# Kernel tuning notes

Measured on AMD Instinct MI355X. Metric: run time of the kernel, lower is better.

The kernel has to match this reference:

```python
import jax, jax.numpy as jnp
import numpy as np
from jax.ops import segment_sum

N = 100000      # nodes
E = 1600000     # edges (avg degree 16)
F_IN = 100      # data.num_features
D1 = 64         # dim1
D2 = 64         # dim2
CONV = 4        # conv_count
FC = 2          # fc_count
G = 500         # graphs in batch


def setup_inputs() -> dict:
    key = jax.random.key(0)
    ks = jax.random.split(key, 16)
    inp = {}
    inp['x'] = jax.random.normal(ks[0], (N, F_IN), dtype=jnp.float32)
    inp['edge_index'] = jax.random.randint(ks[1], (2, E), 0, N, dtype=jnp.int64)
    inp['edge_weight'] = jax.random.uniform(ks[2], (E,), dtype=jnp.float32)
    inp['batch'] = jnp.sort(jax.random.randint(ks[3], (N,), 0, G, dtype=jnp.int64))
    s = 0.05
    inp['lin0_w'] = jax.random.normal(ks[4], (F_IN, D1), dtype=jnp.float32) * s
    inp['lin0_b'] = jnp.zeros((D1,), dtype=jnp.float32)
    inp['conv_w'] = jax.random.normal(ks[5], (CONV, D1, D1), dtype=jnp.float32) * s
    inp['conv_b'] = jnp.zeros((CONV, D1), dtype=jnp.float32)
    inp['lin1_w'] = jax.random.normal(ks[6], (D1, D2), dtype=jnp.float32) * s
    inp['lin1_b'] = jnp.zeros((D2,), dtype=jnp.float32)
    inp['fc_w'] = jax.random.normal(ks[7], (FC, D2, D2), dtype=jnp.float32) * s
    inp['fc_b'] = jnp.zeros((FC, D2), dtype=jnp.float32)
    inp['lin2_w'] = jax.random.normal(ks[8], (D2, 1), dtype=jnp.float32) * s
    inp['lin2_b'] = jnp.zeros((1,), dtype=jnp.float32)
    return inp


def reference(x, edge_index, edge_weight, batch,
              lin0_w, lin0_b, conv_w, conv_b,
              lin1_w, lin1_b, fc_w, fc_b, lin2_w, lin2_b):
    row, col = edge_index[0], edge_index[1]  # source -> target

    # GCN symmetric normalization (add_self_loops=False, so 'improved' is a no-op)
    deg = segment_sum(edge_weight, col, num_segments=N)          # [N]
    dis = jnp.where(deg > 0, jax.lax.rsqrt(deg), 0.0)            # deg^{-1/2}, inf->0
    norm = dis[row] * edge_weight * dis[col]                     # [E]

    out = jax.nn.relu(x @ lin0_w + lin0_b)                       # [N, D1]
    for i in range(CONV):
        h = out @ conv_w[i]                                      # [N, D1]
        msg = h[row] * norm[:, None]                             # gather + scale, [E, D1]
        agg = segment_sum(msg, col, num_segments=N)              # scatter-add, [N, D1]
        out = jax.nn.relu(agg + conv_b[i])

    # global_mean_pool over graph ids
    sums = segment_sum(out, batch, num_segments=G)               # [G, D1]
    cnt = segment_sum(jnp.ones((N,), dtype=out.dtype), batch, num_segments=G)
    pooled = sums / jnp.clip(cnt, 1.0)[:, None]

    out = jax.nn.relu(pooled @ lin1_w + lin1_b)                  # [G, D2]
    for i in range(FC):
        out = jax.nn.relu(out @ fc_w[i] + fc_b[i])
    out = out @ lin2_w + lin2_b                                  # [G, 1]
    return out.reshape(-1)                                       # [G]
```

## Files before the change

### kernel.cpp

```cpp
#include <hip/hip_runtime.h>

#define NN 100000
#define NE 1600000
#define FIN 100
#define D 64
#define NCONV 4
#define NG 500

#define NB 196
#define BSH 9
#define EPB 2048
#define NBLKA ((NE + EPB - 1) / EPB)
#define NSCAN (NB * NBLKA)
#define SB 512
#define NBLKS ((NSCAN + SB - 1) / SB)

#define LSTR 136
#define ASTR 72

typedef unsigned int uint;
typedef unsigned short ushort;
typedef __attribute__((ext_vector_type(8))) short bf16x8;
typedef __attribute__((ext_vector_type(4))) float f32x4;

__device__ inline ushort f2bf(float x) {
    uint u = __float_as_uint(x);
    u += 0x7fffu + ((u >> 16) & 1u);
    return (ushort)(u >> 16);
}
__device__ inline float bflo(uint u) { return __uint_as_float(u << 16); }
__device__ inline float bfhi(uint u) { return __uint_as_float(u & 0xffff0000u); }
__device__ inline float bf2f(ushort s) { return __uint_as_float((uint)s << 16); }

__global__ __launch_bounds__(256) void k_hist(const int* __restrict__ col,
                                              int* __restrict__ ghist) {
    __shared__ int lh[NB];
    int t = threadIdx.x;
    if (t < NB) lh[t] = 0;
    __syncthreads();
    int base = blockIdx.x * EPB;
    #pragma unroll
    for (int i = 0; i < 8; ++i) {
        int e = base + i * 256 + t;
        if (e < NE) atomicAdd(&lh[col[e] >> BSH], 1);
    }
    __syncthreads();
    if (t < NB) ghist[t * NBLKA + blockIdx.x] = lh[t];
}

__global__ __launch_bounds__(SB) void s_scan1(const int* __restrict__ in,
                                              int* __restrict__ out,
                                              int* __restrict__ bsums, int n) {
    __shared__ int sh[SB];
    int t = threadIdx.x, i = blockIdx.x * SB + t;
    int v = (i < n) ? in[i] : 0;
    sh[t] = v;
    __syncthreads();
    for (int off = 1; off < SB; off <<= 1) {
        int u = (t >= off) ? sh[t - off] : 0;
        __syncthreads();
        sh[t] += u;
        __syncthreads();
    }
    if (i < n) out[i] = sh[t] - v;
    if (t == SB - 1) bsums[blockIdx.x] = sh[t];
}

__global__ __launch_bounds__(SB) void s_scan2(int* __restrict__ bsums, int nb) {
    __shared__ int sh[SB];
    int t = threadIdx.x;
    int v = (t < nb) ? bsums[t] : 0;
    sh[t] = v;
    __syncthreads();
    for (int off = 1; off < SB; off <<= 1) {
        int u = (t >= off) ? sh[t - off] : 0;
        __syncthreads();
        sh[t] += u;
        __syncthreads();
    }
    if (t < nb) bsums[t] = sh[t] - v;
}

__global__ __launch_bounds__(SB) void s_scan3(int* __restrict__ out,
                                              const int* __restrict__ bsums, int n) {
    int i = blockIdx.x * SB + threadIdx.x;
    if (i < n) out[i] += bsums[blockIdx.x];
}

__global__ __launch_bounds__(256) void k_scatter(const int* __restrict__ row,
                                                 const int* __restrict__ col,
                                                 const float* __restrict__ ew,
                                                 const int* __restrict__ gscan,
                                                 int2* __restrict__ sorted) {
    __shared__ int lcur[NB];
    int t = threadIdx.x;
    if (t < NB) lcur[t] = gscan[t * NBLKA + blockIdx.x];
    __syncthreads();
    int base = blockIdx.x * EPB;
    #pragma unroll
    for (int i = 0; i < 8; ++i) {
        int e = base + i * 256 + t;
        if (e < NE) {
            int c = col[e];
            int pos = atomicAdd(&lcur[c >> BSH], 1);
            sorted[pos] = make_int2(row[e] | ((c & 511) << 17), __float_as_int(ew[e]));
        }
    }
}

__global__ __launch_bounds__(SB) void k_bcsr(const int2* __restrict__ sorted,
                                             const int* __restrict__ gscan,
                                             int* __restrict__ rowstart,
                                             int2* __restrict__ csr) {
    __shared__ int lcnt[SB];
    __shared__ int lscan[SB];
    int t = threadIdx.x, b = blockIdx.x;
    int base = gscan[b * NBLKA];
    int end  = (b == NB - 1) ? NE : gscan[(b + 1) * NBLKA];
    lcnt[t] = 0;
    __syncthreads();
    for (int e = base + t; e < end; e += SB)
        atomicAdd(&lcnt[sorted[e].x >> 17], 1);
    __syncthreads();
    int v = lcnt[t];
    lscan[t] = v;
    __syncthreads();
    for (int off = 1; off < SB; off <<= 1) {
        int u = (t >= off) ? lscan[t - off] : 0;
        __syncthreads();
        lscan[t] += u;
        __syncthreads();
    }
    int ex = lscan[t] - v;
    int idx = b * SB + t;
    if (idx <= NN) rowstart[idx] = base + ex;
    lcnt[t] = base + ex;
    __syncthreads();
    for (int e = base + t; e < end; e += SB) {
        int2 p = sorted[e];
        int slot = atomicAdd(&lcnt[p.x >> 17], 1);
        csr[slot] = make_int2(p.x & 0x1FFFF, p.y);
    }
}

__global__ __launch_bounds__(256) void k_rowdeg(const int2* __restrict__ csr,
                                                const int* __restrict__ rowstart,
                                                float* __restrict__ dis) {
    int t = threadIdx.x;
    int node = blockIdx.x * 16 + (t >> 4);
    int f = t & 15;
    int e0 = rowstart[node], e1 = rowstart[node + 1];
    float d = 0.f;
    for (int e = e0 + f; e < e1; e += 16) d += __int_as_float(csr[e].y);
    d += __shfl_xor(d, 1);
    d += __shfl_xor(d, 2);
    d += __shfl_xor(d, 4);
    d += __shfl_xor(d, 8);
    if (f == 0) dis[node] = (d > 0.f) ? (1.0f / sqrtf(d)) : 0.f;
}

__global__ __launch_bounds__(256) void k_rownorm(int2* __restrict__ csr,
                                                 const int* __restrict__ rowstart,
                                                 const float* __restrict__ dis) {
    int t = threadIdx.x;
    int node = blockIdx.x * 16 + (t >> 4);
    int f = t & 15;
    int e0 = rowstart[node], e1 = rowstart[node + 1];
    float dc = dis[node];
    for (int e = e0 + f; e < e1; e += 16) {
        int2 p = csr[e];
        float w = dis[p.x] * __int_as_float(p.y) * dc;
        csr[e] = make_int2(p.x, __float_as_int(w));
    }
}

__global__ void k_wsplit(const float* __restrict__ conv_w, ushort* __restrict__ wf) {
    int tid = blockIdx.x * blockDim.x + threadIdx.x;
    int j = tid & 7;
    int lane = (tid >> 3) & 63;
    int kh = (tid >> 9) & 1;
    int ct = (tid >> 10) & 3;
    int l = tid >> 12;
    int k = kh * 32 + (lane >> 4) * 8 + j;
    int n = ct * 16 + (lane & 15);
    float w = conv_w[l * D * D + k * D + n];
    ushort hi = f2bf(w);
    ushort lo = f2bf(w - bf2f(hi));
    int base = (((l * 4 + ct) * 2 + kh) * 2) * 512 + lane * 8 + j;
    wf[base] = hi;
    wf[base + 512] = lo;
}

__global__ void k_wsplit0(const float* __restrict__ w, ushort* __restrict__ wf) {
    int tid = blockIdx.x * blockDim.x + threadIdx.x;
    int j = tid & 7;
    int lane = (tid >> 3) & 63;
    int ks = (tid >> 9) & 3;
    int ct = tid >> 11;
    int k = ks * 32 + (lane >> 4) * 8 + j;
    int n = ct * 16 + (lane & 15);
    float v = (k < FIN) ? w[k * D + n] : 0.f;
    ushort hi = f2bf(v);
    ushort lo = f2bf(v - bf2f(hi));
    int base = ((ct * 4 + ks) * 2) * 512 + lane * 8 + j;
    wf[base] = hi;
    wf[base + 512] = lo;
}

__global__ __launch_bounds__(256) void k_lin0_mfma(const float* __restrict__ x,
                                                   const ushort* __restrict__ wf,
                                                   const float* __restrict__ b,
                                                   ushort* __restrict__ out) {
    __shared__ ushort xhi[64 * LSTR];
    __shared__ ushort xlo[64 * LSTR];
    int t = threadIdx.x;
    int r0 = blockIdx.x * 64;
    for (int i = t; i < 1600; i += 256) {
        int r = i / 25, c4 = i - (i / 25) * 25;
        float4 v = {0.f, 0.f, 0.f, 0.f};
        if (r0 + r < NN)
            v = *reinterpret_cast<const float4*>(&x[(size_t)(r0 + r) * FIN + c4 * 4]);
        int base = r * LSTR + c4 * 4;
        ushort h;
        h = f2bf(v.x); xhi[base + 0] = h; xlo[base + 0] = f2bf(v.x - bf2f(h));
        h = f2bf(v.y); xhi[base + 1] = h; xlo[base + 1] = f2bf(v.y - bf2f(h));
        h = f2bf(v.z); xhi[base + 2] = h; xlo[base + 2] = f2bf(v.z - bf2f(h));
        h = f2bf(v.w); xhi[base + 3] = h; xlo[base + 3] = f2bf(v.w - bf2f(h));
    }
    for (int i = t; i < 64 * 28; i += 256) {
        int r = i / 28, c = FIN + (i - (i / 28) * 28);
        xhi[r * LSTR + c] = 0;
        xlo[r * LSTR + c] = 0;
    }
    __syncthreads();
    int wave = t >> 6, lane = t & 63;
    int lrow = wave * 16 + (lane & 15);
    bf16x8 ahi[4], alo[4];
    #pragma unroll
    for (int ks = 0; ks < 4; ++ks) {
        int off = lrow * LSTR + ks * 32 + (lane >> 4) * 8;
        ahi[ks] = *reinterpret_cast<const bf16x8*>(&xhi[off]);
        alo[ks] = *reinterpret_cast<const bf16x8*>(&xlo[off]);
    }
    float bv[4];
    #pragma unroll
    for (int ct = 0; ct < 4; ++ct) bv[ct] = b[ct * 16 + (lane & 15)];
    int r = r0 + wave * 16;
    f32x4 acc[4];
    #pragma unroll
    for (int ct = 0; ct < 4; ++ct) {
        acc[ct] = {bv[ct], bv[ct], bv[ct], bv[ct]};
        #pragma unroll
        for (int ks = 0; ks < 4; ++ks) {
            int base = ((ct * 4 + ks) * 2) * 512 + lane * 8;
            bf16x8 wh = *reinterpret_cast<const bf16x8*>(&wf[base]);
            bf16x8 wl = *reinterpret_cast<const bf16x8*>(&wf[base + 512]);
            acc[ct] = __builtin_amdgcn_mfma_f32_16x16x32_bf16(ahi[ks], wh, acc[ct], 0, 0, 0);
            acc[ct] = __builtin_amdgcn_mfma_f32_16x16x32_bf16(ahi[ks], wl, acc[ct], 0, 0, 0);
            acc[ct] = __builtin_amdgcn_mfma_f32_16x16x32_bf16(alo[ks], wh, acc[ct], 0, 0, 0);
        }
    }
    #pragma unroll
    for (int ct = 0; ct < 4; ++ct) {
        int ocol = ct * 16 + (lane & 15);
        #pragma unroll
        for (int i = 0; i < 4; ++i) {
            int orow = r + (lane >> 4) * 4 + i;
            if (orow < NN) out[orow * D + ocol] = f2bf(fmaxf(acc[ct][i], 0.f));
        }
    }
}

__global__ __launch_bounds__(256, 8) void k_conv_fused(const ushort* __restrict__ src,
                                                       const int* __restrict__ rowstart,
                                                       const int2* __restrict__ csr,
                                                       const ushort* __restrict__ wf,
                                                       const float* __restrict__ bias,
                                                       ushort* __restrict__ dst) {
    __shared__ ushort arow[16 * ASTR];
    int t = threadIdx.x;
    int wave = t >> 6, lane = t & 63;
    int g = lane >> 4;
    int f = lane & 15;
    int rloc = wave * 4 + g;
    int node = blockIdx.x * 16 + rloc;
    int e0 = rowstart[node], e1 = rowstart[node + 1];
    float4 acc = {0.f, 0.f, 0.f, 0.f};
    int2 p0, p1, p2, p3;
    {
        int a0 = e0 + 0 < e1 ? e0 + 0 : 0;
        int a1 = e0 + 1 < e1 ? e0 + 1 : 0;
        int a2 = e0 + 2 < e1 ? e0 + 2 : 0;
        int a3 = e0 + 3 < e1 ? e0 + 3 : 0;
        p0 = csr[a0]; p1 = csr[a1]; p2 = csr[a2]; p3 = csr[a3];
    }
    for (int base = e0; base < e1; base += 4) {
        int n0 = base + 4 < e1 ? base + 4 : 0;
        int n1 = base + 5 < e1 ? base + 5 : 0;
        int n2 = base + 6 < e1 ? base + 6 : 0;
        int n3 = base + 7 < e1 ? base + 7 : 0;
        int2 q0 = csr[n0], q1 = csr[n1], q2 = csr[n2], q3 = csr[n3];
        float w0 = (base + 0 < e1) ? __int_as_float(p0.y) : 0.f;
        float w1 = (base + 1 < e1) ? __int_as_float(p1.y) : 0.f;
        float w2 = (base + 2 < e1) ? __int_as_float(p2.y) : 0.f;
        float w3 = (base + 3 < e1) ? __int_as_float(p3.y) : 0.f;
        uint2 v0 = *reinterpret_cast<const uint2*>(&src[p0.x * D + f * 4]);
        uint2 v1 = *reinterpret_cast<const uint2*>(&src[p1.x * D + f * 4]);
        uint2 v2 = *reinterpret_cast<const uint2*>(&src[p2.x * D + f * 4]);
        uint2 v3 = *reinterpret_cast<const uint2*>(&src[p3.x * D + f * 4]);
        acc.x = fmaf(bflo(v0.x), w0, acc.x); acc.y = fmaf(bfhi(v0.x), w0, acc.y);
        acc.z = fmaf(bflo(v0.y), w0, acc.z); acc.w = fmaf(bfhi(v0.y), w0, acc.w);
        acc.x = fmaf(bflo(v1.x), w1, acc.x); acc.y = fmaf(bfhi(v1.x), w1, acc.y);
        acc.z = fmaf(bflo(v1.y), w1, acc.z); acc.w = fmaf(bfhi(v1.y), w1, acc.w);
        acc.x = fmaf(bflo(v2.x), w2, acc.x); acc.y = fmaf(bfhi(v2.x), w2, acc.y);
        acc.z = fmaf(bflo(v2.y), w2, acc.z); acc.w = fmaf(bfhi(v2.y), w2, acc.w);
        acc.x = fmaf(bflo(v3.x), w3, acc.x); acc.y = fmaf(bfhi(v3.x), w3, acc.y);
        acc.z = fmaf(bflo(v3.y), w3, acc.z); acc.w = fmaf(bfhi(v3.y), w3, acc.w);
        p0 = q0; p1 = q1; p2 = q2; p3 = q3;
    }
    uint2 o;
    o.x = (uint)f2bf(acc.x) | ((uint)f2bf(acc.y) << 16);
    o.y = (uint)f2bf(acc.z) | ((uint)f2bf(acc.w) << 16);
    *reinterpret_cast<uint2*>(&arow[rloc * ASTR + f * 4]) = o;
    __syncthreads();
    int ct = wave;
    int base0 = ((ct * 2 + 0) * 2) * 512 + lane * 8;
    int base1 = ((ct * 2 + 1) * 2) * 512 + lane * 8;
    bf16x8 wh0 = *reinterpret_cast<const bf16x8*>(&wf[base0]);
    bf16x8 wl0 = *reinterpret_cast<const bf16x8*>(&wf[base0 + 512]);
    bf16x8 wh1 = *reinterpret_cast<const bf16x8*>(&wf[base1]);
    bf16x8 wl1 = *reinterpret_cast<const bf16x8*>(&wf[base1 + 512]);
    int arow_idx = lane & 15;
    bf16x8 a0 = *reinterpret_cast<const bf16x8*>(&arow[arow_idx * ASTR + (lane >> 4) * 8]);
    bf16x8 a1 = *reinterpret_cast<const bf16x8*>(&arow[arow_idx * ASTR + 32 + (lane >> 4) * 8]);
    float bv = bias[ct * 16 + (lane & 15)];
    f32x4 c = {bv, bv, bv, bv};
    c = __builtin_amdgcn_mfma_f32_16x16x32_bf16(a0, wh0, c, 0, 0, 0);
    c = __builtin_amdgcn_mfma_f32_16x16x32_bf16(a1, wh1, c, 0, 0, 0);
    c = __builtin_amdgcn_mfma_f32_16x16x32_bf16(a0, wl0, c, 0, 0, 0);
    c = __builtin_amdgcn_mfma_f32_16x16x32_bf16(a1, wl1, c, 0, 0, 0);
    int ocol = ct * 16 + (lane & 15);
    int r0 = blockIdx.x * 16;
    #pragma unroll
    for (int i = 0; i < 4; ++i) {
        int orow = r0 + (lane >> 4) * 4 + i;
        dst[orow * D + ocol] = f2bf(fmaxf(c[i], 0.f));
    }
}

__global__ __launch_bounds__(256) void k_pool(const ushort* __restrict__ src,
                                              const int* __restrict__ batch,
                                              float* __restrict__ pooled,
                                              float* __restrict__ cnt) {
    int wave = threadIdx.x >> 6, lane = threadIdx.x & 63;
    int n0 = blockIdx.x * 64 + wave * 16;
    float s = 0.f;
    int curg = -1, runlen = 0;
    for (int i = 0; i < 16; ++i) {
        int node = n0 + i;
        if (node >= NN) break;
        int gg = batch[node];
        if (gg != curg) {
            if (curg >= 0) {
                atomicAdd(&pooled[curg * D + lane], s);
                if (lane == 0) atomicAdd(&cnt[curg], (float)runlen);
            }
            curg = gg; s = 0.f; runlen = 0;
        }
        s += bf2f(src[node * D + lane]);
        ++runlen;
    }
    if (curg >= 0) {
        atomicAdd(&pooled[curg * D + lane], s);
        if (lane == 0) atomicAdd(&cnt[curg], (float)runlen);
    }
}

__global__ __launch_bounds__(64) void k_head(const float* __restrict__ pooled,
                                             const float* __restrict__ cnt,
                                             const float* __restrict__ lin1_w,
                                             const float* __restrict__ lin1_b,
                                             const float* __restrict__ fc_w,
                                             const float* __restrict__ fc_b,
                                             const float* __restrict__ lin2_w,
                                             const float* __restrict__ lin2_b,
                                             float* __restrict__ out) {
    __shared__ float buf0[D], buf1[D];
    int g = blockIdx.x, d = threadIdx.x;
    float c = fmaxf(cnt[g], 1.0f);
    buf0[d] = pooled[g * D + d] / c;
    __syncthreads();
    float acc = lin1_b[d];
    #pragma unroll
    for (int k = 0; k < D; ++k) acc += buf0[k] * lin1_w[k * D + d];
    buf1[d] = fmaxf(acc, 0.f);
    __syncthreads();
    acc = fc_b[d];
    #pragma unroll
    for (int k = 0; k < D; ++k) acc += buf1[k] * fc_w[k * D + d];
    buf0[d] = fmaxf(acc, 0.f);
    __syncthreads();
    acc = fc_b[D + d];
    #pragma unroll
    for (int k = 0; k < D; ++k) acc += buf0[k] * fc_w[D * D + k * D + d];
    buf1[d] = fmaxf(acc, 0.f);
    __syncthreads();
    float v = buf1[d] * lin2_w[d];
    #pragma unroll
    for (int off = 32; off; off >>= 1) v += __shfl_down(v, off);
    if (d == 0) out[g] = v + lin2_b[0];
}

extern "C" void kernel_launch(void* const* d_in, const int* in_sizes, int n_in,
                              void* d_out, int out_size, void* d_ws, size_t ws_size,
                              hipStream_t stream) {
    const float* x      = (const float*)d_in[0];
    const int*   ei     = (const int*)  d_in[1];
    const float* ew     = (const float*)d_in[2];
    const int*   batch  = (const int*)  d_in[3];
    const float* lin0_w = (const float*)d_in[4];
    const float* lin0_b = (const float*)d_in[5];
    const float* conv_w = (const float*)d_in[6];
    const float* conv_b = (const float*)d_in[7];
    const float* lin1_w = (const float*)d_in[8];
    const float* lin1_b = (const float*)d_in[9];
    const float* fc_w   = (const float*)d_in[10];
    const float* fc_b   = (const float*)d_in[11];
    const float* lin2_w = (const float*)d_in[12];
    const float* lin2_b = (const float*)d_in[13];
    float* out = (float*)d_out;

    const int* rowv = ei;
    const int* colv = ei + NE;

    ushort* bufA    = (ushort*)d_ws;
    ushort* bufB    = bufA + (size_t)NN * D;
    ushort* bufG    = bufB + (size_t)NN * D;
    int2*   csr     = (int2*)(bufG + (size_t)NN * D);
    int*   rowstart = (int*)(csr + NE);
    float* dis      = (float*)(rowstart + NN + 1);
    float* pooled   = dis + NN;
    float* cnt      = pooled + NG * D;
    ushort* wfrags  = (ushort*)(cnt + NG);
    ushort* wfrags0 = wfrags + 4 * 8192;
    int2*  sorted   = (int2*)bufG;
    int*   ghist    = (int*)bufB;
    int*   gscan    = ghist + NSCAN;
    int*   bsums    = gscan + NSCAN;

    hipMemsetAsync(pooled, 0, (NG * D + NG) * sizeof(float), stream);

    k_hist<<<NBLKA, 256, 0, stream>>>(colv, ghist);
    s_scan1<<<NBLKS, SB, 0, stream>>>(ghist, gscan, bsums, NSCAN);
    s_scan2<<<1, SB, 0, stream>>>(bsums, NBLKS);
    s_scan3<<<NBLKS, SB, 0, stream>>>(gscan, bsums, NSCAN);
    k_scatter<<<NBLKA, 256, 0, stream>>>(rowv, colv, ew, gscan, sorted);
    k_bcsr<<<NB, SB, 0, stream>>>(sorted, gscan, rowstart, csr);

    k_rowdeg<<<NN / 16, 256, 0, stream>>>(csr, rowstart, dis);
    k_rownorm<<<NN / 16, 256, 0, stream>>>(csr, rowstart, dis);
    k_wsplit<<<64, 256, 0, stream>>>(conv_w, wfrags);
    k_wsplit0<<<32, 256, 0, stream>>>(lin0_w, wfrags0);

    k_lin0_mfma<<<(NN + 63) / 64, 256, 0, stream>>>(x, wfrags0, lin0_b, bufA);

    int cg = NN / 16;
    k_conv_fused<<<cg, 256, 0, stream>>>(bufA, rowstart, csr, wfrags + 0 * 8192,
                                         conv_b + 0 * D, bufB);
    k_conv_fused<<<cg, 256, 0, stream>>>(bufB, rowstart, csr, wfrags + 1 * 8192,
                                         conv_b + 1 * D, bufA);
    k_conv_fused<<<cg, 256, 0, stream>>>(bufA, rowstart, csr, wfrags + 2 * 8192,
                                         conv_b + 2 * D, bufB);
    k_conv_fused<<<cg, 256, 0, stream>>>(bufB, rowstart, csr, wfrags + 3 * 8192,
                                         conv_b + 3 * D, bufA);

    k_pool<<<(NN + 63) / 64, 256, 0, stream>>>(bufA, batch, pooled, cnt);
    k_head<<<NG, 64, 0, stream>>>(pooled, cnt, lin1_w, lin1_b, fc_w, fc_b,
                                  lin2_w, lin2_b, out);
}
```

Measured before the change: 280.1 us.

## Fuse degree into CSR build, merge weight splits, drop x low part, per-wave conv tiles

Computes the degree normalisation inside the bucket-CSR kernel using shared-memory float atomics, which removes the separate row-degree kernel. The two weight-split kernels are merged into one launch, and the edge-bucketing kernels now handle 4096 edges per block. lin0 drops the low bf16 half of x, saving one MFMA and the shared-memory buffer per product but lowering precision. The conv kernel now has each wave own 16 nodes and all four output column tiles, so blocks cover 64 nodes with no block-level barrier, at the cost of redundant weight loads per wave.

```diff
diff --git a/kernel.cpp b/kernel.cpp
--- a/kernel.cpp
+++ b/kernel.cpp
@@ -9,7 +9,7 @@
 
 #define NB 196
 #define BSH 9
-#define EPB 2048
+#define EPB 4096
 #define NBLKA ((NE + EPB - 1) / EPB)
 #define NSCAN (NB * NBLKA)
 #define SB 512
@@ -40,7 +40,7 @@
     __syncthreads();
     int base = blockIdx.x * EPB;
     #pragma unroll
-    for (int i = 0; i < 8; ++i) {
+    for (int i = 0; i < 16; ++i) {
         int e = base + i * 256 + t;
         if (e < NE) atomicAdd(&lh[col[e] >> BSH], 1);
     }
@@ -98,7 +98,7 @@
     __syncthreads();
     int base = blockIdx.x * EPB;
     #pragma unroll
-    for (int i = 0; i < 8; ++i) {
+    for (int i = 0; i < 16; ++i) {
         int e = base + i * 256 + t;
         if (e < NE) {
             int c = col[e];
@@ -111,16 +111,23 @@
 __global__ __launch_bounds__(SB) void k_bcsr(const int2* __restrict__ sorted,
                                              const int* __restrict__ gscan,
                                              int* __restrict__ rowstart,
-                                             int2* __restrict__ csr) {
+                                             int2* __restrict__ csr,
+                                             float* __restrict__ dis) {
     __shared__ int lcnt[SB];
     __shared__ int lscan[SB];
+    __shared__ float ldeg[SB];
     int t = threadIdx.x, b = blockIdx.x;
     int base = gscan[b * NBLKA];
     int end  = (b == NB - 1) ? NE : gscan[(b + 1) * NBLKA];
     lcnt[t] = 0;
-    __syncthreads();
-    for (int e = base + t; e < end; e += SB)
-        atomicAdd(&lcnt[sorted[e].x >> 17], 1);
+    ldeg[t] = 0.f;
+    __syncthreads();
+    for (int e = base + t; e < end; e += SB) {
+        int2 p = sorted[e];
+        int c = p.x >> 17;
+        atomicAdd(&lcnt[c], 1);
+        atomicAdd(&ldeg[c], __int_as_float(p.y));
+    }
     __syncthreads();
     int v = lcnt[t];
     lscan[t] = v;
@@ -134,6 +141,10 @@
     int ex = lscan[t] - v;
     int idx = b * SB + t;
     if (idx <= NN) rowstart[idx] = base + ex;
+    if (idx < NN) {
+        float dd = ldeg[t];
+        dis[idx] = (dd > 0.f) ? (1.0f / sqrtf(dd)) : 0.f;
+    }
     lcnt[t] = base + ex;
     __syncthreads();
     for (int e = base + t; e < end; e += SB) {
@@ -141,22 +152,6 @@
         int slot = atomicAdd(&lcnt[p.x >> 17], 1);
         csr[slot] = make_int2(p.x & 0x1FFFF, p.y);
     }
-}
-
-__global__ __launch_bounds__(256) void k_rowdeg(const int2* __restrict__ csr,
-                                                const int* __restrict__ rowstart,
-                                                float* __restrict__ dis) {
-    int t = threadIdx.x;
-    int node = blockIdx.x * 16 + (t >> 4);
-    int f = t & 15;
-    int e0 = rowstart[node], e1 = rowstart[node + 1];
-    float d = 0.f;
-    for (int e = e0 + f; e < e1; e += 16) d += __int_as_float(csr[e].y);
-    d += __shfl_xor(d, 1);
-    d += __shfl_xor(d, 2);
-    d += __shfl_xor(d, 4);
-    d += __shfl_xor(d, 8);
-    if (f == 0) dis[node] = (d > 0.f) ? (1.0f / sqrtf(d)) : 0.f;
 }
 
 __global__ __launch_bounds__(256) void k_rownorm(int2* __restrict__ csr,
@@ -174,37 +169,39 @@
     }
 }
 
-__global__ void k_wsplit(const float* __restrict__ conv_w, ushort* __restrict__ wf) {
+__global__ void k_wsplit_all(const float* __restrict__ conv_w,
+                             const float* __restrict__ lin0_w,
+                             ushort* __restrict__ wf, ushort* __restrict__ wf0) {
     int tid = blockIdx.x * blockDim.x + threadIdx.x;
-    int j = tid & 7;
-    int lane = (tid >> 3) & 63;
-    int kh = (tid >> 9) & 1;
-    int ct = (tid >> 10) & 3;
-    int l = tid >> 12;
-    int k = kh * 32 + (lane >> 4) * 8 + j;
-    int n = ct * 16 + (lane & 15);
-    float w = conv_w[l * D * D + k * D + n];
-    ushort hi = f2bf(w);
-    ushort lo = f2bf(w - bf2f(hi));
-    int base = (((l * 4 + ct) * 2 + kh) * 2) * 512 + lane * 8 + j;
-    wf[base] = hi;
-    wf[base + 512] = lo;
-}
-
-__global__ void k_wsplit0(const float* __restrict__ w, ushort* __restrict__ wf) {
-    int tid = blockIdx.x * blockDim.x + threadIdx.x;
-    int j = tid & 7;
-    int lane = (tid >> 3) & 63;
-    int ks = (tid >> 9) & 3;
-    int ct = tid >> 11;
-    int k = ks * 32 + (lane >> 4) * 8 + j;
-    int n = ct * 16 + (lane & 15);
-    float v = (k < FIN) ? w[k * D + n] : 0.f;
-    ushort hi = f2bf(v);
-    ushort lo = f2bf(v - bf2f(hi));
-    int base = ((ct * 4 + ks) * 2) * 512 + lane * 8 + j;
-    wf[base] = hi;
-    wf[base + 512] = lo;
+    if (tid < 16384) {
+        int j = tid & 7;
+        int lane = (tid >> 3) & 63;
+        int kh = (tid >> 9) & 1;
+        int ct = (tid >> 10) & 3;
+        int l = tid >> 12;
+        int k = kh * 32 + (lane >> 4) * 8 + j;
+        int n = ct * 16 + (lane & 15);
+        float w = conv_w[l * D * D + k * D + n];
+        ushort hi = f2bf(w);
+        ushort lo = f2bf(w - bf2f(hi));
+        int base = (((l * 4 + ct) * 2 + kh) * 2) * 512 + lane * 8 + j;
+        wf[base] = hi;
+        wf[base + 512] = lo;
+    } else {
+        int s = tid - 16384;
+        int j = s & 7;
+        int lane = (s >> 3) & 63;
+        int ks = (s >> 9) & 3;
+        int ct = s >> 11;
+        int k = ks * 32 + (lane >> 4) * 8 + j;
+        int n = ct * 16 + (lane & 15);
+        float v = (k < FIN) ? lin0_w[k * D + n] : 0.f;
+        ushort hi = f2bf(v);
+        ushort lo = f2bf(v - bf2f(hi));
+        int base = ((ct * 4 + ks) * 2) * 512 + lane * 8 + j;
+        wf0[base] = hi;
+        wf0[base + 512] = lo;
+    }
 }
 
 __global__ __launch_bounds__(256) void k_lin0_mfma(const float* __restrict__ x,
@@ -212,7 +209,6 @@
                                                    const float* __restrict__ b,
                                                    ushort* __restrict__ out) {
     __shared__ ushort xhi[64 * LSTR];
-    __shared__ ushort xlo[64 * LSTR];
     int t = threadIdx.x;
     int r0 = blockIdx.x * 64;
     for (int i = t; i < 1600; i += 256) {
@@ -221,26 +217,23 @@
         if (r0 + r < NN)
             v = *reinterpret_cast<const float4*>(&x[(size_t)(r0 + r) * FIN + c4 * 4]);
         int base = r * LSTR + c4 * 4;
-        ushort h;
-        h = f2bf(v.x); xhi[base + 0] = h; xlo[base + 0] = f2bf(v.x - bf2f(h));
-        h = f2bf(v.y); xhi[base + 1] = h; xlo[base + 1] = f2bf(v.y - bf2f(h));
-        h = f2bf(v.z); xhi[base + 2] = h; xlo[base + 2] = f2bf(v.z - bf2f(h));
-        h = f2bf(v.w); xhi[base + 3] = h; xlo[base + 3] = f2bf(v.w - bf2f(h));
+        xhi[base + 0] = f2bf(v.x);
+        xhi[base + 1] = f2bf(v.y);
+        xhi[base + 2] = f2bf(v.z);
+        xhi[base + 3] = f2bf(v.w);
     }
     for (int i = t; i < 64 * 28; i += 256) {
         int r = i / 28, c = FIN + (i - (i / 28) * 28);
         xhi[r * LSTR + c] = 0;
-        xlo[r * LSTR + c] = 0;
     }
     __syncthreads();
     int wave = t >> 6, lane = t & 63;
     int lrow = wave * 16 + (lane & 15);
-    bf16x8 ahi[4], alo[4];
+    bf16x8 ahi[4];
     #pragma unroll
     for (int ks = 0; ks < 4; ++ks) {
         int off = lrow * LSTR + ks * 32 + (lane >> 4) * 8;
         ahi[ks] = *reinterpret_cast<const bf16x8*>(&xhi[off]);
-        alo[ks] = *reinterpret_cast<const bf16x8*>(&xlo[off]);
     }
     float bv[4];
     #pragma unroll
@@ -257,7 +250,6 @@
             bf16x8 wl = *reinterpret_cast<const bf16x8*>(&wf[base + 512]);
             acc[ct] = __builtin_amdgcn_mfma_f32_16x16x32_bf16(ahi[ks], wh, acc[ct], 0, 0, 0);
             acc[ct] = __builtin_amdgcn_mfma_f32_16x16x32_bf16(ahi[ks], wl, acc[ct], 0, 0, 0);
-            acc[ct] = __builtin_amdgcn_mfma_f32_16x16x32_bf16(alo[ks], wh, acc[ct], 0, 0, 0);
         }
     }
     #pragma unroll
@@ -277,74 +269,81 @@
                                                        const ushort* __restrict__ wf,
                                                        const float* __restrict__ bias,
                                                        ushort* __restrict__ dst) {
-    __shared__ ushort arow[16 * ASTR];
+    __shared__ ushort arow[4][16 * ASTR];
     int t = threadIdx.x;
     int wave = t >> 6, lane = t & 63;
     int g = lane >> 4;
     int f = lane & 15;
-    int rloc = wave * 4 + g;
-    int node = blockIdx.x * 16 + rloc;
-    int e0 = rowstart[node], e1 = rowstart[node + 1];
-    float4 acc = {0.f, 0.f, 0.f, 0.f};
-    int2 p0, p1, p2, p3;
-    {
-        int a0 = e0 + 0 < e1 ? e0 + 0 : 0;
-        int a1 = e0 + 1 < e1 ? e0 + 1 : 0;
-        int a2 = e0 + 2 < e1 ? e0 + 2 : 0;
-        int a3 = e0 + 3 < e1 ? e0 + 3 : 0;
-        p0 = csr[a0]; p1 = csr[a1]; p2 = csr[a2]; p3 = csr[a3];
-    }
-    for (int base = e0; base < e1; base += 4) {
-        int n0 = base + 4 < e1 ? base + 4 : 0;
-        int n1 = base + 5 < e1 ? base + 5 : 0;
-        int n2 = base + 6 < e1 ? base + 6 : 0;
-        int n3 = base + 7 < e1 ? base + 7 : 0;
-        int2 q0 = csr[n0], q1 = csr[n1], q2 = csr[n2], q3 = csr[n3];
-        float w0 = (base + 0 < e1) ? __int_as_float(p0.y) : 0.f;
-        float w1 = (base + 1 < e1) ? __int_as_float(p1.y) : 0.f;
-        float w2 = (base + 2 < e1) ? __int_as_float(p2.y) : 0.f;
-        float w3 = (base + 3 < e1) ? __int_as_float(p3.y) : 0.f;
-        uint2 v0 = *reinterpret_cast<const uint2*>(&src[p0.x * D + f * 4]);
-        uint2 v1 = *reinterpret_cast<const uint2*>(&src[p1.x * D + f * 4]);
-        uint2 v2 = *reinterpret_cast<const uint2*>(&src[p2.x * D + f * 4]);
-        uint2 v3 = *reinterpret_cast<const uint2*>(&src[p3.x * D + f * 4]);
-        acc.x = fmaf(bflo(v0.x), w0, acc.x); acc.y = fmaf(bfhi(v0.x), w0, acc.y);
-        acc.z = fmaf(bflo(v0.y), w0, acc.z); acc.w = fmaf(bfhi(v0.y), w0, acc.w);
-        acc.x = fmaf(bflo(v1.x), w1, acc.x); acc.y = fmaf(bfhi(v1.x), w1, acc.y);
-        acc.z = fmaf(bflo(v1.y), w1, acc.z); acc.w = fmaf(bfhi(v1.y), w1, acc.w);
-        acc.x = fmaf(bflo(v2.x), w2, acc.x); acc.y = fmaf(bfhi(v2.x), w2, acc.y);
-        acc.z = fmaf(bflo(v2.y), w2, acc.z); acc.w = fmaf(bfhi(v2.y), w2, acc.w);
-        acc.x = fmaf(bflo(v3.x), w3, acc.x); acc.y = fmaf(bfhi(v3.x), w3, acc.y);
-        acc.z = fmaf(bflo(v3.y), w3, acc.z); acc.w = fmaf(bfhi(v3.y), w3, acc.w);
-        p0 = q0; p1 = q1; p2 = q2; p3 = q3;
-    }
-    uint2 o;
-    o.x = (uint)f2bf(acc.x) | ((uint)f2bf(acc.y) << 16);
-    o.y = (uint)f2bf(acc.z) | ((uint)f2bf(acc.w) << 16);
-    *reinterpret_cast<uint2*>(&arow[rloc * ASTR + f * 4]) = o;
-    __syncthreads();
-    int ct = wave;
-    int base0 = ((ct * 2 + 0) * 2) * 512 + lane * 8;
-    int base1 = ((ct * 2 + 1) * 2) * 512 + lane * 8;
-    bf16x8 wh0 = *reinterpret_cast<const bf16x8*>(&wf[base0]);
-    bf16x8 wl0 = *reinterpret_cast<const bf16x8*>(&wf[base0 + 512]);
-    bf16x8 wh1 = *reinterpret_cast<const bf16x8*>(&wf[base1]);
-    bf16x8 wl1 = *reinterpret_cast<const bf16x8*>(&wf[base1 + 512]);
+    int n0 = blockIdx.x * 64 + wave * 16;
+    if (n0 >= NN) return;
+    ushort* tile = arow[wave];
+
+    #pragma unroll
+    for (int p = 0; p < 4; ++p) {
+        int rloc = p * 4 + g;
+        int node = n0 + rloc;
+        int e0 = rowstart[node], e1 = rowstart[node + 1];
+        float4 acc = {0.f, 0.f, 0.f, 0.f};
+        int2 p0, p1, p2, p3;
+        {
+            int a0 = e0 + 0 < e1 ? e0 + 0 : 0;
+            int a1 = e0 + 1 < e1 ? e0 + 1 : 0;
+            int a2 = e0 + 2 < e1 ? e0 + 2 : 0;
+            int a3 = e0 + 3 < e1 ? e0 + 3 : 0;
+            p0 = csr[a0]; p1 = csr[a1]; p2 = csr[a2]; p3 = csr[a3];
+        }
+        for (int base = e0; base < e1; base += 4) {
+            int n0e = base + 4 < e1 ? base + 4 : 0;
+            int n1e = base + 5 < e1 ? base + 5 : 0;
+            int n2e = base + 6 < e1 ? base + 6 : 0;
+            int n3e = base + 7 < e1 ? base + 7 : 0;
+            int2 q0 = csr[n0e], q1 = csr[n1e], q2 = csr[n2e], q3 = csr[n3e];
+            float w0 = (base + 0 < e1) ? __int_as_float(p0.y) : 0.f;
+            float w1 = (base + 1 < e1) ? __int_as_float(p1.y) : 0.f;
+            float w2 = (base + 2 < e1) ? __int_as_float(p2.y) : 0.f;
+            float w3 = (base + 3 < e1) ? __int_as_float(p3.y) : 0.f;
+            uint2 v0 = *reinterpret_cast<const uint2*>(&src[p0.x * D + f * 4]);
+            uint2 v1 = *reinterpret_cast<const uint2*>(&src[p1.x * D + f * 4]);
+            uint2 v2 = *reinterpret_cast<const uint2*>(&src[p2.x * D + f * 4]);
+            uint2 v3 = *reinterpret_cast<const uint2*>(&src[p3.x * D + f * 4]);
+            acc.x = fmaf(bflo(v0.x), w0, acc.x); acc.y = fmaf(bfhi(v0.x), w0, acc.y);
+            acc.z = fmaf(bflo(v0.y), w0, acc.z); acc.w = fmaf(bfhi(v0.y), w0, acc.w);
+            acc.x = fmaf(bflo(v1.x), w1, acc.x); acc.y = fmaf(bfhi(v1.x), w1, acc.y);
+            acc.z = fmaf(bflo(v1.y), w1, acc.z); acc.w = fmaf(bfhi(v1.y), w1, acc.w);
+            acc.x = fmaf(bflo(v2.x), w2, acc.x); acc.y = fmaf(bfhi(v2.x), w2, acc.y);
+            acc.z = fmaf(bflo(v2.y), w2, acc.z); acc.w = fmaf(bfhi(v2.y), w2, acc.w);
+            acc.x = fmaf(bflo(v3.x), w3, acc.x); acc.y = fmaf(bfhi(v3.x), w3, acc.y);
+            acc.z = fmaf(bflo(v3.y), w3, acc.z); acc.w = fmaf(bfhi(v3.y), w3, acc.w);
+            p0 = q0; p1 = q1; p2 = q2; p3 = q3;
+        }
+        uint2 o;
+        o.x = (uint)f2bf(acc.x) | ((uint)f2bf(acc.y) << 16);
+        o.y = (uint)f2bf(acc.z) | ((uint)f2bf(acc.w) << 16);
+        *reinterpret_cast<uint2*>(&tile[rloc * ASTR + f * 4]) = o;
+    }
     int arow_idx = lane & 15;
-    bf16x8 a0 = *reinterpret_cast<const bf16x8*>(&arow[arow_idx * ASTR + (lane >> 4) * 8]);
-    bf16x8 a1 = *reinterpret_cast<const bf16x8*>(&arow[arow_idx * ASTR + 32 + (lane >> 4) * 8]);
-    float bv = bias[ct * 16 + (lane & 15)];
-    f32x4 c = {bv, bv, bv, bv};
-    c = __builtin_amdgcn_mfma_f32_16x16x32_bf16(a0, wh0, c, 0, 0, 0);
-    c = __builtin_amdgcn_mfma_f32_16x16x32_bf16(a1, wh1, c, 0, 0, 0);
-    c = __builtin_amdgcn_mfma_f32_16x16x32_bf16(a0, wl0, c, 0, 0, 0);
-    c = __builtin_amdgcn_mfma_f32_16x16x32_bf16(a1, wl1, c, 0, 0, 0);
-    int ocol = ct * 16 + (lane & 15);
-    int r0 = blockIdx.x * 16;
-    #pragma unroll
-    for (int i = 0; i < 4; ++i) {
-        int orow = r0 + (lane >> 4) * 4 + i;
-        dst[orow * D + ocol] = f2bf(fmaxf(c[i], 0.f));
+    bf16x8 a0 = *reinterpret_cast<const bf16x8*>(&tile[arow_idx * ASTR + (lane >> 4) * 8]);
+    bf16x8 a1 = *reinterpret_cast<const bf16x8*>(&tile[arow_idx * ASTR + 32 + (lane >> 4) * 8]);
+    #pragma unroll
+    for (int ct = 0; ct < 4; ++ct) {
+        int base0 = ((ct * 2 + 0) * 2) * 512 + lane * 8;
+        int base1 = ((ct * 2 + 1) * 2) * 512 + lane * 8;
+        bf16x8 wh0 = *reinterpret_cast<const bf16x8*>(&wf[base0]);
+        bf16x8 wl0 = *reinterpret_cast<const bf16x8*>(&wf[base0 + 512]);
+        bf16x8 wh1 = *reinterpret_cast<const bf16x8*>(&wf[base1]);
+        bf16x8 wl1 = *reinterpret_cast<const bf16x8*>(&wf[base1 + 512]);
+        float bv = bias[ct * 16 + (lane & 15)];
+        f32x4 c = {bv, bv, bv, bv};
+        c = __builtin_amdgcn_mfma_f32_16x16x32_bf16(a0, wh0, c, 0, 0, 0);
+        c = __builtin_amdgcn_mfma_f32_16x16x32_bf16(a1, wh1, c, 0, 0, 0);
+        c = __builtin_amdgcn_mfma_f32_16x16x32_bf16(a0, wl0, c, 0, 0, 0);
+        c = __builtin_amdgcn_mfma_f32_16x16x32_bf16(a1, wl1, c, 0, 0, 0);
+        int ocol = ct * 16 + (lane & 15);
+        #pragma unroll
+        for (int i = 0; i < 4; ++i) {
+            int orow = n0 + (lane >> 4) * 4 + i;
+            dst[orow * D + ocol] = f2bf(fmaxf(c[i], 0.f));
+        }
     }
 }
 
@@ -455,16 +454,14 @@
     s_scan2<<<1, SB, 0, stream>>>(bsums, NBLKS);
     s_scan3<<<NBLKS, SB, 0, stream>>>(gscan, bsums, NSCAN);
     k_scatter<<<NBLKA, 256, 0, stream>>>(rowv, colv, ew, gscan, sorted);
-    k_bcsr<<<NB, SB, 0, stream>>>(sorted, gscan, rowstart, csr);
-
-    k_rowdeg<<<NN / 16, 256, 0, stream>>>(csr, rowstart, dis);
+    k_bcsr<<<NB, SB, 0, stream>>>(sorted, gscan, rowstart, csr, dis);
+
     k_rownorm<<<NN / 16, 256, 0, stream>>>(csr, rowstart, dis);
-    k_wsplit<<<64, 256, 0, stream>>>(conv_w, wfrags);
-    k_wsplit0<<<32, 256, 0, stream>>>(lin0_w, wfrags0);
+    k_wsplit_all<<<96, 256, 0, stream>>>(conv_w, lin0_w, wfrags, wfrags0);
 
     k_lin0_mfma<<<(NN + 63) / 64, 256, 0, stream>>>(x, wfrags0, lin0_b, bufA);
 
-    int cg = NN / 16;
+    int cg = (NN + 63) / 64;
     k_conv_fused<<<cg, 256, 0, stream>>>(bufA, rowstart, csr, wfrags + 0 * 8192,
                                          conv_b + 0 * D, bufB);
     k_conv_fused<<<cg, 256, 0, stream>>>(bufB, rowstart, csr, wfrags + 1 * 8192,
```

New measurement: 311.0 us. 1.11x slower.
